# Kernel optimization log

Hardware: AMD Instinct MI355X
Metric: run time of the kernel (lower is better)

Reference implementation:

```python
import jax, jax.numpy as jnp
import numpy as np

N = 50000      # nodes
E = 800000     # directed edges
D = 128        # input_dim == hidden_dim
EL = 100000    # edges scored by decoder


def setup_inputs() -> dict:
    key = jax.random.key(0)
    ks = jax.random.split(key, 8)
    s = 1.0 / np.sqrt(D)  # glorot-ish scale
    return {
        "node_feature": jax.random.normal(ks[0], (N, D), jnp.float32),
        "W1": jax.random.normal(ks[1], (D, D), jnp.float32) * s,
        "b1": jnp.zeros((D,), jnp.float32),
        "W2": jax.random.normal(ks[2], (D, D), jnp.float32) * s,
        "b2": jnp.zeros((D,), jnp.float32),
        "W3": jax.random.normal(ks[3], (D, D), jnp.float32) * s,
        "b3": jnp.zeros((D,), jnp.float32),
        "edge_index": jax.random.randint(ks[4], (2, E), 0, N, dtype=jnp.int32),
        "edge_label_index": jax.random.randint(ks[5], (2, EL), 0, N, dtype=jnp.int32),
    }


def _gcn_conv(x, W, b, src, dst, norm, n):
    # x' = D^{-1/2} (A + I) D^{-1/2} (x W) + b   (PyG GCNConv semantics)
    h = x @ W                                   # [N, D]
    msg = h[src] * norm[:, None]                # gather + scale, [E+N, D]
    out = jax.ops.segment_sum(msg, dst, num_segments=n)  # scatter-add
    return out + b


def reference(node_feature, W1, b1, W2, b2, W3, b3, edge_index, edge_label_index):
    n = node_feature.shape[0]
    loop = jnp.arange(n, dtype=edge_index.dtype)
    src = jnp.concatenate([edge_index[0], loop])  # self-loops appended
    dst = jnp.concatenate([edge_index[1], loop])
    # symmetric normalization: deg over destinations (incl. self-loops)
    deg = jax.ops.segment_sum(jnp.ones_like(dst, dtype=node_feature.dtype), dst, num_segments=n)
    dinv = jax.lax.rsqrt(jnp.maximum(deg, 1.0))
    norm = dinv[src] * dinv[dst]                 # [E+N]

    x = jax.nn.relu(_gcn_conv(node_feature, W1, b1, src, dst, norm, n))
    x = jax.nn.relu(_gcn_conv(x, W2, b2, src, dst, norm, n))
    x = _gcn_conv(x, W3, b3, src, dst, norm, n)

    # dot-product edge decoder
    u = x[edge_label_index[0]]
    v = x[edge_label_index[1]]
    return jnp.sum(u * v, axis=-1)               # [EL] logits
```

## Files before the change

kernel.cpp:

```cpp
#include <hip/hip_runtime.h>
#include <hip/hip_bf16.h>
#include <hip/hip_fp16.h>

typedef _Float16 v8h __attribute__((ext_vector_type(8)));
typedef _Float16 v4h __attribute__((ext_vector_type(4)));
typedef float v4f __attribute__((ext_vector_type(4)));

__global__ __launch_bounds__(256) void hist_wswz(const int* __restrict__ dst,
                                                 int* __restrict__ histT, int E,
                                                 int histBlocks,
                                                 const float* __restrict__ W1,
                                                 const float* __restrict__ W2,
                                                 const float* __restrict__ W3,
                                                 __half* __restrict__ wfrag) {
    int tid = threadIdx.x;
    if (blockIdx.x >= histBlocks) {
        int o = (blockIdx.x - histBlocks) * 256 + tid;
        int w = o >> 14, r = o & 16383;
        const float* Ws = (w >= 3) ? W3 : ((w == 2) ? W2 : W1);
        float v = Ws[r];
        __half h;
        if (w == 1) {
            __half hv = __float2half_rn(v);
            h = __float2half_rn(v - __half2float(hv));
        } else {
            h = __float2half_rn(v);
        }
        int k = r >> 7, ncol = r & 127;
        int c = ncol >> 4, nl = ncol & 15;
        int s = k >> 5, quad = (k >> 3) & 3, j = k & 7;
        int di = ((c * 4 + s) * 64 + quad * 16 + nl) * 8 + j;
        wfrag[(size_t)w * 16384 + di] = h;
        return;
    }
    __shared__ int h[256];
    h[tid] = 0;
    __syncthreads();
    int base = blockIdx.x * 2048 + tid * 8;
    if (base + 7 < E) {
        int4 d0 = *(const int4*)&dst[base];
        int4 d1 = *(const int4*)&dst[base + 4];
        atomicAdd(&h[d0.x >> 8], 1);
        atomicAdd(&h[d0.y >> 8], 1);
        atomicAdd(&h[d0.z >> 8], 1);
        atomicAdd(&h[d0.w >> 8], 1);
        atomicAdd(&h[d1.x >> 8], 1);
        atomicAdd(&h[d1.y >> 8], 1);
        atomicAdd(&h[d1.z >> 8], 1);
        atomicAdd(&h[d1.w >> 8], 1);
    } else {
        for (int e = base; e < E; ++e) atomicAdd(&h[dst[e] >> 8], 1);
    }
    __syncthreads();
    histT[tid * 400 + blockIdx.x] = h[tid];
}

__global__ __launch_bounds__(512) void scan_bins(int* __restrict__ histT,
                                                 int* __restrict__ totals, int nb) {
    __shared__ int s[512];
    int b = blockIdx.x;
    int t = threadIdx.x;
    int v = (t < nb) ? histT[b * 400 + t] : 0;
    s[t] = v;
    __syncthreads();
    for (int off = 1; off < 512; off <<= 1) {
        int x = (t >= off) ? s[t - off] : 0;
        __syncthreads();
        s[t] += x;
        __syncthreads();
    }
    if (t < nb) histT[b * 400 + t] = s[t] - v;
    if (t == 511) totals[b] = s[511];
}

__global__ __launch_bounds__(256) void scan_totals(const int* __restrict__ totals,
                                                   int* __restrict__ binbase) {
    __shared__ int s[256];
    int t = threadIdx.x;
    int v = totals[t];
    s[t] = v;
    __syncthreads();
    for (int off = 1; off < 256; off <<= 1) {
        int x = (t >= off) ? s[t - off] : 0;
        __syncthreads();
        s[t] += x;
        __syncthreads();
    }
    binbase[t] = s[t] - v;
    if (t == 255) binbase[256] = s[255];
}

__global__ __launch_bounds__(256) void scat_gemm1(const int* __restrict__ src,
                                                  const int* __restrict__ dst,
                                                  const int* __restrict__ histT,
                                                  const int* __restrict__ binbase,
                                                  int* __restrict__ pairS, int E,
                                                  int scatBlocks,
                                                  const float* __restrict__ X,
                                                  const __half* __restrict__ wfrag,
                                                  __half* __restrict__ H, int Nrows) {
    int tid = threadIdx.x;
    if (blockIdx.x < scatBlocks) {
        __shared__ int pos[256];
        pos[tid] = binbase[tid] + histT[tid * 400 + blockIdx.x];
        __syncthreads();
        int base = blockIdx.x * 2048 + tid * 8;
        if (base + 7 < E) {
            int4 d0 = *(const int4*)&dst[base];
            int4 d1 = *(const int4*)&dst[base + 4];
            int4 s0 = *(const int4*)&src[base];
            int4 s1 = *(const int4*)&src[base + 4];
            int p0 = atomicAdd(&pos[d0.x >> 8], 1);
            int p1 = atomicAdd(&pos[d0.y >> 8], 1);
            int p2 = atomicAdd(&pos[d0.z >> 8], 1);
            int p3 = atomicAdd(&pos[d0.w >> 8], 1);
            int p4 = atomicAdd(&pos[d1.x >> 8], 1);
            int p5 = atomicAdd(&pos[d1.y >> 8], 1);
            int p6 = atomicAdd(&pos[d1.z >> 8], 1);
            int p7 = atomicAdd(&pos[d1.w >> 8], 1);
            pairS[p0] = ((d0.x & 255) << 16) | s0.x;
            pairS[p1] = ((d0.y & 255) << 16) | s0.y;
            pairS[p2] = ((d0.z & 255) << 16) | s0.z;
            pairS[p3] = ((d0.w & 255) << 16) | s0.w;
            pairS[p4] = ((d1.x & 255) << 16) | s1.x;
            pairS[p5] = ((d1.y & 255) << 16) | s1.y;
            pairS[p6] = ((d1.z & 255) << 16) | s1.z;
            pairS[p7] = ((d1.w & 255) << 16) | s1.w;
        } else {
            for (int e = base; e < E; ++e) {
                int d = dst[e];
                int p = atomicAdd(&pos[d >> 8], 1);
                pairS[p] = ((d & 255) << 16) | src[e];
            }
        }
        return;
    }
    int rowbase = (blockIdx.x - scatBlocks) * 64;
    int l = tid & 63;
    int wid = tid >> 6;
    int rb = wid * 16;
    int quad = l >> 4;
    int nn = l & 15;
    int gr = rowbase + rb + nn;
    v8h ah[4], al[4];
    if (gr < Nrows) {
        const float* Xr = &X[(size_t)gr * 128 + quad * 8];
#pragma unroll
        for (int k = 0; k < 4; ++k) {
            float4 f0 = *(const float4*)&Xr[k * 32];
            float4 f1 = *(const float4*)&Xr[k * 32 + 4];
            float ff[8] = {f0.x, f0.y, f0.z, f0.w, f1.x, f1.y, f1.z, f1.w};
            v8h h, lo;
#pragma unroll
            for (int m = 0; m < 8; ++m) {
                _Float16 hv = (_Float16)ff[m];
                h[m] = hv;
                lo[m] = (_Float16)(ff[m] - (float)hv);
            }
            ah[k] = h;
            al[k] = lo;
        }
    } else {
#pragma unroll
        for (int k = 0; k < 4; ++k) {
            v8h z;
#pragma unroll
            for (int m = 0; m < 8; ++m) z[m] = (_Float16)0.f;
            ah[k] = z;
            al[k] = z;
        }
    }
    const v8h* Wh = (const v8h*)wfrag;
    const v8h* Wl = (const v8h*)(wfrag + 16384);
    v4f acc[8] = {};
    v8h bh0 = Wh[0 * 64 + l];
    v8h bh1 = Wh[1 * 64 + l];
    v8h bh2 = Wh[2 * 64 + l];
    v8h bh3 = Wh[3 * 64 + l];
#pragma unroll
    for (int c = 0; c < 8; ++c) {
        v8h bl0 = Wl[(c * 4 + 0) * 64 + l];
        v8h bl1 = Wl[(c * 4 + 1) * 64 + l];
        v8h bl2 = Wl[(c * 4 + 2) * 64 + l];
        v8h bl3 = Wl[(c * 4 + 3) * 64 + l];
        acc[c] = __builtin_amdgcn_mfma_f32_16x16x32_f16(ah[0], bh0, acc[c], 0, 0, 0);
        acc[c] = __builtin_amdgcn_mfma_f32_16x16x32_f16(ah[1], bh1, acc[c], 0, 0, 0);
        acc[c] = __builtin_amdgcn_mfma_f32_16x16x32_f16(ah[2], bh2, acc[c], 0, 0, 0);
        acc[c] = __builtin_amdgcn_mfma_f32_16x16x32_f16(ah[3], bh3, acc[c], 0, 0, 0);
        acc[c] = __builtin_amdgcn_mfma_f32_16x16x32_f16(al[0], bh0, acc[c], 0, 0, 0);
        acc[c] = __builtin_amdgcn_mfma_f32_16x16x32_f16(al[1], bh1, acc[c], 0, 0, 0);
        acc[c] = __builtin_amdgcn_mfma_f32_16x16x32_f16(al[2], bh2, acc[c], 0, 0, 0);
        acc[c] = __builtin_amdgcn_mfma_f32_16x16x32_f16(al[3], bh3, acc[c], 0, 0, 0);
        v8h nh0, nh1, nh2, nh3;
        if (c < 7) {
            nh0 = Wh[((c + 1) * 4 + 0) * 64 + l];
            nh1 = Wh[((c + 1) * 4 + 1) * 64 + l];
            nh2 = Wh[((c + 1) * 4 + 2) * 64 + l];
            nh3 = Wh[((c + 1) * 4 + 3) * 64 + l];
        }
        acc[c] = __builtin_amdgcn_mfma_f32_16x16x32_f16(ah[0], bl0, acc[c], 0, 0, 0);
        acc[c] = __builtin_amdgcn_mfma_f32_16x16x32_f16(ah[1], bl1, acc[c], 0, 0, 0);
        acc[c] = __builtin_amdgcn_mfma_f32_16x16x32_f16(ah[2], bl2, acc[c], 0, 0, 0);
        acc[c] = __builtin_amdgcn_mfma_f32_16x16x32_f16(ah[3], bl3, acc[c], 0, 0, 0);
        if (c < 7) { bh0 = nh0; bh1 = nh1; bh2 = nh2; bh3 = nh3; }
    }
#pragma unroll
    for (int reg = 0; reg < 4; ++reg) {
        int grr = rowbase + rb + quad * 4 + reg;
        if (grr < Nrows) {
#pragma unroll
            for (int c = 0; c < 8; ++c)
                H[(size_t)grr * 128 + c * 16 + nn] = __float2half_rn(acc[c][reg]);
        }
    }
}

__global__ __launch_bounds__(256) void bucket_csr(const int* __restrict__ pairS,
                                                  const int* __restrict__ binbase,
                                                  int* __restrict__ rowptr,
                                                  float* __restrict__ dinv,
                                                  int* __restrict__ col, int N) {
    __shared__ int h[256];
    __shared__ int sc[256];
    __shared__ int cnt2[256];
    int b = blockIdx.x;
    int t = threadIdx.x;
    int ebeg = binbase[b], eend = binbase[b + 1];
    int base_sl = ebeg + b * 256;
    h[t] = 0;
    __syncthreads();
    for (int i = ebeg + t; i < eend; i += 256) atomicAdd(&h[pairS[i] >> 16], 1);
    __syncthreads();
    int deg = h[t];
    int node = b * 256 + t;
    bool valid = node < N;
    int v = valid ? (deg + 1) : 0;
    sc[t] = v;
    __syncthreads();
    for (int off = 1; off < 256; off <<= 1) {
        int x = (t >= off) ? sc[t - off] : 0;
        __syncthreads();
        sc[t] += x;
        __syncthreads();
    }
    int rs = base_sl + sc[t] - v;
    if (valid) {
        rowptr[node + 1] = base_sl + sc[t];
        dinv[node] = rsqrtf((float)(deg + 1));
        col[rs] = node;
        if (node == 0) rowptr[0] = 0;
    }
    cnt2[t] = rs + 1;
    __syncthreads();
    for (int i = ebeg + t; i < eend; i += 256) {
        int pv = pairS[i];
        int p = atomicAdd(&cnt2[pv >> 16], 1);
        col[p] = pv & 0xFFFF;
    }
}

__global__ __launch_bounds__(512, 8) void agg_gemm(const __half* __restrict__ Xs,
                                                   const float* __restrict__ dinv,
                                                   const int* __restrict__ rowptr,
                                                   const int* __restrict__ col,
                                                   const __half* __restrict__ wfrag,
                                                   const float* __restrict__ bias,
                                                   __half* __restrict__ Out,
                                                   int n, int finalLayer) {
    __shared__ __align__(16) _Float16 y[64][136];
    int tid = threadIdx.x;
    int rowbase = blockIdx.x * 64;
    {
        int grp = tid >> 4;
        int t = (tid & 15) * 8;
        for (int g = 0; g < 2; ++g) {
            int rr = g * 32 + grp;
            int node = rowbase + rr;
            float a[8] = {};
            if (node < n) {
                int beg = rowptr[node], end = rowptr[node + 1];
                int k = beg;
                for (; k + 4 <= end; k += 4) {
                    int s0 = col[k], s1 = col[k + 1], s2 = col[k + 2], s3 = col[k + 3];
                    uint4 r0 = *(const uint4*)&Xs[(size_t)s0 * 128 + t];
                    uint4 r1 = *(const uint4*)&Xs[(size_t)s1 * 128 + t];
                    uint4 r2 = *(const uint4*)&Xs[(size_t)s2 * 128 + t];
                    uint4 r3 = *(const uint4*)&Xs[(size_t)s3 * 128 + t];
                    const __half2* h0 = (const __half2*)&r0;
                    const __half2* h1 = (const __half2*)&r1;
                    const __half2* h2 = (const __half2*)&r2;
                    const __half2* h3 = (const __half2*)&r3;
#pragma unroll
                    for (int m = 0; m < 4; ++m) {
                        float2 f0 = __half22float2(h0[m]);
                        float2 f1 = __half22float2(h1[m]);
                        float2 f2 = __half22float2(h2[m]);
                        float2 f3 = __half22float2(h3[m]);
                        a[2 * m]     += (f0.x + f1.x) + (f2.x + f3.x);
                        a[2 * m + 1] += (f0.y + f1.y) + (f2.y + f3.y);
                    }
                }
                for (; k < end; ++k) {
                    uint4 r0 = *(const uint4*)&Xs[(size_t)col[k] * 128 + t];
                    const __half2* h0 = (const __half2*)&r0;
#pragma unroll
                    for (int m = 0; m < 4; ++m) {
                        float2 f0 = __half22float2(h0[m]);
                        a[2 * m] += f0.x;
                        a[2 * m + 1] += f0.y;
                    }
                }
                float dn = dinv[node];
#pragma unroll
                for (int m = 0; m < 8; ++m) a[m] *= dn;
            }
            v8h yv;
#pragma unroll
            for (int m = 0; m < 8; ++m) yv[m] = (_Float16)a[m];
            *(v8h*)&y[rr][t] = yv;
        }
    }
    __syncthreads();
    int l = tid & 63;
    int wid = tid >> 6;
    int rb = (wid >> 1) * 16;
    int ch = wid & 1;
    int quad = l >> 4;
    int nn = l & 15;
    v8h a0 = *(const v8h*)&y[rb + nn][0 * 32 + quad * 8];
    v8h a1 = *(const v8h*)&y[rb + nn][1 * 32 + quad * 8];
    v8h a2 = *(const v8h*)&y[rb + nn][2 * 32 + quad * 8];
    v8h a3 = *(const v8h*)&y[rb + nn][3 * 32 + quad * 8];
    const v8h* Wf = (const v8h*)wfrag;
    v4f acc[4] = {};
#pragma unroll
    for (int c = 0; c < 4; ++c) {
        int cc = ch * 4 + c;
        v8h b0 = Wf[(cc * 4 + 0) * 64 + l];
        v8h b1 = Wf[(cc * 4 + 1) * 64 + l];
        v8h b2 = Wf[(cc * 4 + 2) * 64 + l];
        v8h b3 = Wf[(cc * 4 + 3) * 64 + l];
        acc[c] = __builtin_amdgcn_mfma_f32_16x16x32_f16(a0, b0, acc[c], 0, 0, 0);
        acc[c] = __builtin_amdgcn_mfma_f32_16x16x32_f16(a1, b1, acc[c], 0, 0, 0);
        acc[c] = __builtin_amdgcn_mfma_f32_16x16x32_f16(a2, b2, acc[c], 0, 0, 0);
        acc[c] = __builtin_amdgcn_mfma_f32_16x16x32_f16(a3, b3, acc[c], 0, 0, 0);
    }
#pragma unroll
    for (int reg = 0; reg < 4; ++reg) {
        int gr = rowbase + rb + quad * 4 + reg;
        if (gr < n) {
            float dn = dinv[gr];
#pragma unroll
            for (int c = 0; c < 4; ++c) {
                int cc = ch * 4 + c;
                float z = acc[c][reg] + bias[cc * 16 + nn];
                if (!finalLayer) z = fmaxf(z, 0.f) * dn;
                Out[(size_t)gr * 128 + cc * 16 + nn] = __float2half_rn(z);
            }
        }
    }
}

__global__ __launch_bounds__(256, 8) void agg_h(const __half* __restrict__ H,
                                                const float* __restrict__ dinv,
                                                const int* __restrict__ rowptr,
                                                const int* __restrict__ col,
                                                const float* __restrict__ bias,
                                                __half* __restrict__ out, int n) {
    int node = blockIdx.x * 16 + (threadIdx.x >> 4);
    int t = (threadIdx.x & 15) * 8;
    if (node >= n) return;
    int beg = rowptr[node], end = rowptr[node + 1];
    float a[8] = {};
    int k = beg;
    for (; k + 4 <= end; k += 4) {
        int s0 = col[k], s1 = col[k + 1], s2 = col[k + 2], s3 = col[k + 3];
        float w0 = dinv[s0], w1 = dinv[s1], w2 = dinv[s2], w3 = dinv[s3];
        uint4 r0 = *(const uint4*)&H[(size_t)s0 * 128 + t];
        uint4 r1 = *(const uint4*)&H[(size_t)s1 * 128 + t];
        uint4 r2 = *(const uint4*)&H[(size_t)s2 * 128 + t];
        uint4 r3 = *(const uint4*)&H[(size_t)s3 * 128 + t];
        const __half2* h0 = (const __half2*)&r0;
        const __half2* h1 = (const __half2*)&r1;
        const __half2* h2 = (const __half2*)&r2;
        const __half2* h3 = (const __half2*)&r3;
#pragma unroll
        for (int m = 0; m < 4; ++m) {
            float2 f0 = __half22float2(h0[m]);
            float2 f1 = __half22float2(h1[m]);
            float2 f2 = __half22float2(h2[m]);
            float2 f3 = __half22float2(h3[m]);
            a[2 * m]     += f0.x * w0 + f1.x * w1 + f2.x * w2 + f3.x * w3;
            a[2 * m + 1] += f0.y * w0 + f1.y * w1 + f2.y * w2 + f3.y * w3;
        }
    }
    for (; k < end; ++k) {
        int s0 = col[k];
        float w0 = dinv[s0];
        uint4 r0 = *(const uint4*)&H[(size_t)s0 * 128 + t];
        const __half2* h0 = (const __half2*)&r0;
#pragma unroll
        for (int m = 0; m < 4; ++m) {
            float2 f0 = __half22float2(h0[m]);
            a[2 * m] += f0.x * w0;
            a[2 * m + 1] += f0.y * w0;
        }
    }
    float dn = dinv[node];
    float4 b0 = *(const float4*)&bias[t];
    float4 b1 = *(const float4*)&bias[t + 4];
    float r0 = fmaxf(a[0] * dn + b0.x, 0.f) * dn;
    float r1 = fmaxf(a[1] * dn + b0.y, 0.f) * dn;
    float r2 = fmaxf(a[2] * dn + b0.z, 0.f) * dn;
    float r3 = fmaxf(a[3] * dn + b0.w, 0.f) * dn;
    float r4 = fmaxf(a[4] * dn + b1.x, 0.f) * dn;
    float r5 = fmaxf(a[5] * dn + b1.y, 0.f) * dn;
    float r6 = fmaxf(a[6] * dn + b1.z, 0.f) * dn;
    float r7 = fmaxf(a[7] * dn + b1.w, 0.f) * dn;
    auto pk = [](float x, float y) { __half2 h = __floats2half2_rn(x, y); return *(unsigned int*)&h; };
    uint4 o = make_uint4(pk(r0, r1), pk(r2, r3), pk(r4, r5), pk(r6, r7));
    *(uint4*)&out[(size_t)node * 128 + t] = o;
}

__global__ __launch_bounds__(256) void decoder_h(const __half* __restrict__ X,
                                                 const int* __restrict__ eli,
                                                 float* __restrict__ out, int EL) {
    int e = blockIdx.x * 16 + (threadIdx.x >> 4);
    int lane = threadIdx.x & 15;
    if (e >= EL) return;
    int u = eli[e], v = eli[EL + e];
    uint4 ra = *(const uint4*)&X[(size_t)u * 128 + lane * 8];
    uint4 rb = *(const uint4*)&X[(size_t)v * 128 + lane * 8];
    const __half2* ha = (const __half2*)&ra;
    const __half2* hb = (const __half2*)&rb;
    float d = 0.f;
#pragma unroll
    for (int j = 0; j < 4; ++j) {
        float2 fa = __half22float2(ha[j]);
        float2 fb = __half22float2(hb[j]);
        d += fa.x * fb.x + fa.y * fb.y;
    }
#pragma unroll
    for (int off = 8; off > 0; off >>= 1) d += __shfl_xor(d, off);
    if (lane == 0) out[e] = d;
}

extern "C" void kernel_launch(void* const* d_in, const int* in_sizes, int n_in,
                              void* d_out, int out_size, void* d_ws, size_t ws_size,
                              hipStream_t stream) {
    const float* x0 = (const float*)d_in[0];
    const float* W1 = (const float*)d_in[1];
    const float* b1 = (const float*)d_in[2];
    const float* W2 = (const float*)d_in[3];
    const float* b2 = (const float*)d_in[4];
    const float* W3 = (const float*)d_in[5];
    const float* b3 = (const float*)d_in[6];
    const int* ei   = (const int*)d_in[7];
    const int* eli  = (const int*)d_in[8];
    float* out = (float*)d_out;

    const int D = 128;
    const int N  = in_sizes[0] / D;
    const int E  = in_sizes[7] / 2;
    const int EL = in_sizes[8] / 2;

    const int* src = ei;
    const int* dst = ei + E;

    char* ws = (char*)d_ws;
    size_t off = 0;
    auto alloc = [&](size_t bytes) -> void* {
        off = (off + 255) & ~(size_t)255;
        void* p = ws + off;
        off += bytes;
        return p;
    };
    int*    histT   = (int*)alloc((size_t)256 * 400 * sizeof(int));
    int*    totals  = (int*)alloc(256 * sizeof(int));
    int*    binbase = (int*)alloc(257 * sizeof(int));
    int*    pairS   = (int*)alloc((size_t)E * sizeof(int));
    int*    rowptr  = (int*)alloc((size_t)(N + 1) * sizeof(int));
    float*  dinv    = (float*)alloc((size_t)N * sizeof(float));
    int*    col     = (int*)alloc((size_t)(E + N) * sizeof(int));
    __half* wfrag   = (__half*)alloc((size_t)4 * 16384 * sizeof(__half));
    __half* hbuf    = (__half*)alloc((size_t)N * D * sizeof(__half));
    __half* xbuf    = (__half*)alloc((size_t)N * D * sizeof(__half));
    (void)ws_size;

    int histBlocks = (E + 2047) / 2048;
    int gemmGrid = (N + 63) / 64;
    int fusedGrid = (N + 63) / 64;
    int aggGrid  = (N + 15) / 16;
    int nbkt = (N + 255) / 256;

    hist_wswz<<<histBlocks + 256, 256, 0, stream>>>(dst, histT, E, histBlocks,
                                                    W1, W2, W3, wfrag);
    scan_bins<<<256, 512, 0, stream>>>(histT, totals, histBlocks);
    scan_totals<<<1, 256, 0, stream>>>(totals, binbase);
    scat_gemm1<<<histBlocks + gemmGrid, 256, 0, stream>>>(src, dst, histT, binbase,
                                                          pairS, E, histBlocks,
                                                          x0, wfrag, hbuf, N);
    bucket_csr<<<nbkt, 256, 0, stream>>>(pairS, binbase, rowptr, dinv, col, N);

    agg_h<<<aggGrid, 256, 0, stream>>>(hbuf, dinv, rowptr, col, b1, xbuf, N);
    agg_gemm<<<fusedGrid, 512, 0, stream>>>(xbuf, dinv, rowptr, col, wfrag + 2 * 16384, b2, hbuf, N, 0);
    agg_gemm<<<fusedGrid, 512, 0, stream>>>(hbuf, dinv, rowptr, col, wfrag + 3 * 16384, b3, xbuf, N, 1);

    decoder_h<<<(EL + 15) / 16, 256, 0, stream>>>(xbuf, eli, out, EL);
}
```

Before: 227.9 us.

## Sub-bin edge counting sort by source range within each destination bucket

The counting sort now bins edges by (dst>>8, coarse src range) with 8 source sub-bins per destination bucket, so edges inside each bucket end up partially ordered by source node. Column indices in the CSR should then show better gather locality for the H rows read during aggregation. The cost is an 8x larger histogram and scan (nbins up to about 1600 bins, 2048-entry shared arrays, a 1024-thread totals scan), plus extra src loads in the histogram kernel.

```diff
diff --git a/kernel.cpp b/kernel.cpp
--- a/kernel.cpp
+++ b/kernel.cpp
@@ -3,12 +3,12 @@
 #include <hip/hip_fp16.h>
 
 typedef _Float16 v8h __attribute__((ext_vector_type(8)));
-typedef _Float16 v4h __attribute__((ext_vector_type(4)));
 typedef float v4f __attribute__((ext_vector_type(4)));
 
 __global__ __launch_bounds__(256) void hist_wswz(const int* __restrict__ dst,
+                                                 const int* __restrict__ src,
                                                  int* __restrict__ histT, int E,
-                                                 int histBlocks,
+                                                 int histBlocks, int nbins, int srcShift,
                                                  const float* __restrict__ W1,
                                                  const float* __restrict__ W2,
                                                  const float* __restrict__ W3,
@@ -33,26 +33,29 @@
         wfrag[(size_t)w * 16384 + di] = h;
         return;
     }
-    __shared__ int h[256];
-    h[tid] = 0;
+    __shared__ int h[2048];
+    for (int i = tid; i < nbins; i += 256) h[i] = 0;
     __syncthreads();
     int base = blockIdx.x * 2048 + tid * 8;
     if (base + 7 < E) {
         int4 d0 = *(const int4*)&dst[base];
         int4 d1 = *(const int4*)&dst[base + 4];
-        atomicAdd(&h[d0.x >> 8], 1);
-        atomicAdd(&h[d0.y >> 8], 1);
-        atomicAdd(&h[d0.z >> 8], 1);
-        atomicAdd(&h[d0.w >> 8], 1);
-        atomicAdd(&h[d1.x >> 8], 1);
-        atomicAdd(&h[d1.y >> 8], 1);
-        atomicAdd(&h[d1.z >> 8], 1);
-        atomicAdd(&h[d1.w >> 8], 1);
+        int4 s0 = *(const int4*)&src[base];
+        int4 s1 = *(const int4*)&src[base + 4];
+        atomicAdd(&h[(d0.x >> 8) * 8 + (s0.x >> srcShift)], 1);
+        atomicAdd(&h[(d0.y >> 8) * 8 + (s0.y >> srcShift)], 1);
+        atomicAdd(&h[(d0.z >> 8) * 8 + (s0.z >> srcShift)], 1);
+        atomicAdd(&h[(d0.w >> 8) * 8 + (s0.w >> srcShift)], 1);
+        atomicAdd(&h[(d1.x >> 8) * 8 + (s1.x >> srcShift)], 1);
+        atomicAdd(&h[(d1.y >> 8) * 8 + (s1.y >> srcShift)], 1);
+        atomicAdd(&h[(d1.z >> 8) * 8 + (s1.z >> srcShift)], 1);
+        atomicAdd(&h[(d1.w >> 8) * 8 + (s1.w >> srcShift)], 1);
     } else {
-        for (int e = base; e < E; ++e) atomicAdd(&h[dst[e] >> 8], 1);
-    }
-    __syncthreads();
-    histT[tid * 400 + blockIdx.x] = h[tid];
+        for (int e = base; e < E; ++e)
+            atomicAdd(&h[(dst[e] >> 8) * 8 + (src[e] >> srcShift)], 1);
+    }
+    __syncthreads();
+    for (int i = tid; i < nbins; i += 256) histT[i * 400 + blockIdx.x] = h[i];
 }
 
 __global__ __launch_bounds__(512) void scan_bins(int* __restrict__ histT,
@@ -73,21 +76,26 @@
     if (t == 511) totals[b] = s[511];
 }
 
-__global__ __launch_bounds__(256) void scan_totals(const int* __restrict__ totals,
-                                                   int* __restrict__ binbase) {
-    __shared__ int s[256];
+__global__ __launch_bounds__(1024) void scan_totals(const int* __restrict__ totals,
+                                                    int* __restrict__ binbase, int nbins) {
+    __shared__ int s[1024];
     int t = threadIdx.x;
-    int v = totals[t];
-    s[t] = v;
-    __syncthreads();
-    for (int off = 1; off < 256; off <<= 1) {
+    int CH = (nbins + 1023) >> 10;
+    int beg = t * CH;
+    int end = min(beg + CH, nbins);
+    int sum = 0;
+    for (int i = beg; i < end; ++i) sum += totals[i];
+    s[t] = sum;
+    __syncthreads();
+    for (int off = 1; off < 1024; off <<= 1) {
         int x = (t >= off) ? s[t - off] : 0;
         __syncthreads();
         s[t] += x;
         __syncthreads();
     }
-    binbase[t] = s[t] - v;
-    if (t == 255) binbase[256] = s[255];
+    int run = s[t] - sum;
+    for (int i = beg; i < end; ++i) { binbase[i] = run; run += totals[i]; }
+    if (t == 1023) binbase[nbins] = s[1023];
 }
 
 __global__ __launch_bounds__(256) void scat_gemm1(const int* __restrict__ src,
@@ -95,14 +103,15 @@
                                                   const int* __restrict__ histT,
                                                   const int* __restrict__ binbase,
                                                   int* __restrict__ pairS, int E,
-                                                  int scatBlocks,
+                                                  int scatBlocks, int nbins, int srcShift,
                                                   const float* __restrict__ X,
                                                   const __half* __restrict__ wfrag,
                                                   __half* __restrict__ H, int Nrows) {
     int tid = threadIdx.x;
     if (blockIdx.x < scatBlocks) {
-        __shared__ int pos[256];
-        pos[tid] = binbase[tid] + histT[tid * 400 + blockIdx.x];
+        __shared__ int pos[2048];
+        for (int i = tid; i < nbins; i += 256)
+            pos[i] = binbase[i] + histT[i * 400 + blockIdx.x];
         __syncthreads();
         int base = blockIdx.x * 2048 + tid * 8;
         if (base + 7 < E) {
@@ -110,14 +119,14 @@
             int4 d1 = *(const int4*)&dst[base + 4];
             int4 s0 = *(const int4*)&src[base];
             int4 s1 = *(const int4*)&src[base + 4];
-            int p0 = atomicAdd(&pos[d0.x >> 8], 1);
-            int p1 = atomicAdd(&pos[d0.y >> 8], 1);
-            int p2 = atomicAdd(&pos[d0.z >> 8], 1);
-            int p3 = atomicAdd(&pos[d0.w >> 8], 1);
-            int p4 = atomicAdd(&pos[d1.x >> 8], 1);
-            int p5 = atomicAdd(&pos[d1.y >> 8], 1);
-            int p6 = atomicAdd(&pos[d1.z >> 8], 1);
-            int p7 = atomicAdd(&pos[d1.w >> 8], 1);
+            int p0 = atomicAdd(&pos[(d0.x >> 8) * 8 + (s0.x >> srcShift)], 1);
+            int p1 = atomicAdd(&pos[(d0.y >> 8) * 8 + (s0.y >> srcShift)], 1);
+            int p2 = atomicAdd(&pos[(d0.z >> 8) * 8 + (s0.z >> srcShift)], 1);
+            int p3 = atomicAdd(&pos[(d0.w >> 8) * 8 + (s0.w >> srcShift)], 1);
+            int p4 = atomicAdd(&pos[(d1.x >> 8) * 8 + (s1.x >> srcShift)], 1);
+            int p5 = atomicAdd(&pos[(d1.y >> 8) * 8 + (s1.y >> srcShift)], 1);
+            int p6 = atomicAdd(&pos[(d1.z >> 8) * 8 + (s1.z >> srcShift)], 1);
+            int p7 = atomicAdd(&pos[(d1.w >> 8) * 8 + (s1.w >> srcShift)], 1);
             pairS[p0] = ((d0.x & 255) << 16) | s0.x;
             pairS[p1] = ((d0.y & 255) << 16) | s0.y;
             pairS[p2] = ((d0.z & 255) << 16) | s0.z;
@@ -128,9 +137,9 @@
             pairS[p7] = ((d1.w & 255) << 16) | s1.w;
         } else {
             for (int e = base; e < E; ++e) {
-                int d = dst[e];
-                int p = atomicAdd(&pos[d >> 8], 1);
-                pairS[p] = ((d & 255) << 16) | src[e];
+                int d = dst[e], s = src[e];
+                int p = atomicAdd(&pos[(d >> 8) * 8 + (s >> srcShift)], 1);
+                pairS[p] = ((d & 255) << 16) | s;
             }
         }
         return;
@@ -225,7 +234,7 @@
     __shared__ int cnt2[256];
     int b = blockIdx.x;
     int t = threadIdx.x;
-    int ebeg = binbase[b], eend = binbase[b + 1];
+    int ebeg = binbase[b * 8], eend = binbase[b * 8 + 8];
     int base_sl = ebeg + b * 256;
     h[t] = 0;
     __syncthreads();
@@ -467,6 +476,15 @@
     const int* src = ei;
     const int* dst = ei + E;
 
+    int nbkt = (N + 255) / 256;
+    int nbins = nbkt * 8;
+    int srcShift = 0;
+    while (((N - 1) >> srcShift) >= 8) srcShift++;
+    int histBlocks = (E + 2047) / 2048;
+    int gemmGrid = (N + 63) / 64;
+    int fusedGrid = (N + 63) / 64;
+    int aggGrid  = (N + 15) / 16;
+
     char* ws = (char*)d_ws;
     size_t off = 0;
     auto alloc = [&](size_t bytes) -> void* {
@@ -475,9 +493,9 @@
         off += bytes;
         return p;
     };
-    int*    histT   = (int*)alloc((size_t)256 * 400 * sizeof(int));
-    int*    totals  = (int*)alloc(256 * sizeof(int));
-    int*    binbase = (int*)alloc(257 * sizeof(int));
+    int*    histT   = (int*)alloc((size_t)nbins * 400 * sizeof(int));
+    int*    totals  = (int*)alloc((size_t)nbins * sizeof(int));
+    int*    binbase = (int*)alloc((size_t)(nbins + 1) * sizeof(int));
     int*    pairS   = (int*)alloc((size_t)E * sizeof(int));
     int*    rowptr  = (int*)alloc((size_t)(N + 1) * sizeof(int));
     float*  dinv    = (float*)alloc((size_t)N * sizeof(float));
@@ -487,19 +505,13 @@
     __half* xbuf    = (__half*)alloc((size_t)N * D * sizeof(__half));
     (void)ws_size;
 
-    int histBlocks = (E + 2047) / 2048;
-    int gemmGrid = (N + 63) / 64;
-    int fusedGrid = (N + 63) / 64;
-    int aggGrid  = (N + 15) / 16;
-    int nbkt = (N + 255) / 256;
-
-    hist_wswz<<<histBlocks + 256, 256, 0, stream>>>(dst, histT, E, histBlocks,
-                                                    W1, W2, W3, wfrag);
-    scan_bins<<<256, 512, 0, stream>>>(histT, totals, histBlocks);
-    scan_totals<<<1, 256, 0, stream>>>(totals, binbase);
+    hist_wswz<<<histBlocks + 256, 256, 0, stream>>>(dst, src, histT, E, histBlocks,
+                                                    nbins, srcShift, W1, W2, W3, wfrag);
+    scan_bins<<<nbins, 512, 0, stream>>>(histT, totals, histBlocks);
+    scan_totals<<<1, 1024, 0, stream>>>(totals, binbase, nbins);
     scat_gemm1<<<histBlocks + gemmGrid, 256, 0, stream>>>(src, dst, histT, binbase,
-                                                          pairS, E, histBlocks,
-                                                          x0, wfrag, hbuf, N);
+                                                          pairS, E, histBlocks, nbins,
+                                                          srcShift, x0, wfrag, hbuf, N);
     bucket_csr<<<nbkt, 256, 0, stream>>>(pairS, binbase, rowptr, dinv, col, N);
 
     agg_h<<<aggGrid, 256, 0, stream>>>(hbuf, dinv, rowptr, col, b1, xbuf, N);
```

Result: slower. 238.6 us (+4.7%).

## Remap aggregation to 4 lanes per node looping over feature chunks

Applied to the files above, without the earlier changes.

Both aggregation kernels now give each node 4 threads that loop over four 32-column feature chunks, where before 16 threads covered all 128 columns in one pass. agg_gemm drops to 256 threads per block, and each wave computes all 8 output column tiles for its 16 rows instead of half of them. The aim is to cut per-node thread waste on low-degree rows and to amortize the rowptr/dinv loads. In exchange, each gather now moves only 64 contiguous bytes per node per chunk, the neighbor list is walked four times, and there is less memory-level parallelism per node.

```diff
diff --git a/kernel.cpp b/kernel.cpp
--- a/kernel.cpp
+++ b/kernel.cpp
@@ -3,7 +3,6 @@
 #include <hip/hip_fp16.h>
 
 typedef _Float16 v8h __attribute__((ext_vector_type(8)));
-typedef _Float16 v4h __attribute__((ext_vector_type(4)));
 typedef float v4f __attribute__((ext_vector_type(4)));
 
 __global__ __launch_bounds__(256) void hist_wswz(const int* __restrict__ dst,
@@ -259,7 +258,74 @@
     }
 }
 
-__global__ __launch_bounds__(512, 8) void agg_gemm(const __half* __restrict__ Xs,
+__global__ __launch_bounds__(256, 8) void agg_h(const __half* __restrict__ H,
+                                                const float* __restrict__ dinv,
+                                                const int* __restrict__ rowptr,
+                                                const int* __restrict__ col,
+                                                const float* __restrict__ bias,
+                                                __half* __restrict__ out, int n) {
+    int grp = threadIdx.x >> 2;
+    int lane = threadIdx.x & 3;
+    int node = blockIdx.x * 64 + grp;
+    int beg = 0, end = 0;
+    float dn = 0.f;
+    if (node < n) { beg = rowptr[node]; end = rowptr[node + 1]; dn = dinv[node]; }
+    auto pk = [](float x, float y) { __half2 h = __floats2half2_rn(x, y); return *(unsigned int*)&h; };
+    for (int q = 0; q < 4; ++q) {
+        int t = q * 32 + lane * 8;
+        float a[8] = {};
+        int k = beg;
+        for (; k + 4 <= end; k += 4) {
+            int s0 = col[k], s1 = col[k + 1], s2 = col[k + 2], s3 = col[k + 3];
+            float w0 = dinv[s0], w1 = dinv[s1], w2 = dinv[s2], w3 = dinv[s3];
+            uint4 r0 = *(const uint4*)&H[(size_t)s0 * 128 + t];
+            uint4 r1 = *(const uint4*)&H[(size_t)s1 * 128 + t];
+            uint4 r2 = *(const uint4*)&H[(size_t)s2 * 128 + t];
+            uint4 r3 = *(const uint4*)&H[(size_t)s3 * 128 + t];
+            const __half2* h0 = (const __half2*)&r0;
+            const __half2* h1 = (const __half2*)&r1;
+            const __half2* h2 = (const __half2*)&r2;
+            const __half2* h3 = (const __half2*)&r3;
+#pragma unroll
+            for (int m = 0; m < 4; ++m) {
+                float2 f0 = __half22float2(h0[m]);
+                float2 f1 = __half22float2(h1[m]);
+                float2 f2 = __half22float2(h2[m]);
+                float2 f3 = __half22float2(h3[m]);
+                a[2 * m]     += f0.x * w0 + f1.x * w1 + f2.x * w2 + f3.x * w3;
+                a[2 * m + 1] += f0.y * w0 + f1.y * w1 + f2.y * w2 + f3.y * w3;
+            }
+        }
+        for (; k < end; ++k) {
+            int s0 = col[k];
+            float w0 = dinv[s0];
+            uint4 r0 = *(const uint4*)&H[(size_t)s0 * 128 + t];
+            const __half2* h0 = (const __half2*)&r0;
+#pragma unroll
+            for (int m = 0; m < 4; ++m) {
+                float2 f0 = __half22float2(h0[m]);
+                a[2 * m] += f0.x * w0;
+                a[2 * m + 1] += f0.y * w0;
+            }
+        }
+        if (node < n) {
+            float4 b0 = *(const float4*)&bias[t];
+            float4 b1 = *(const float4*)&bias[t + 4];
+            float r0 = fmaxf(a[0] * dn + b0.x, 0.f) * dn;
+            float r1 = fmaxf(a[1] * dn + b0.y, 0.f) * dn;
+            float r2 = fmaxf(a[2] * dn + b0.z, 0.f) * dn;
+            float r3 = fmaxf(a[3] * dn + b0.w, 0.f) * dn;
+            float r4 = fmaxf(a[4] * dn + b1.x, 0.f) * dn;
+            float r5 = fmaxf(a[5] * dn + b1.y, 0.f) * dn;
+            float r6 = fmaxf(a[6] * dn + b1.z, 0.f) * dn;
+            float r7 = fmaxf(a[7] * dn + b1.w, 0.f) * dn;
+            uint4 o = make_uint4(pk(r0, r1), pk(r2, r3), pk(r4, r5), pk(r6, r7));
+            *(uint4*)&out[(size_t)node * 128 + t] = o;
+        }
+    }
+}
+
+__global__ __launch_bounds__(256, 8) void agg_gemm(const __half* __restrict__ Xs,
                                                    const float* __restrict__ dinv,
                                                    const int* __restrict__ rowptr,
                                                    const int* __restrict__ col,
@@ -271,60 +337,56 @@
     int tid = threadIdx.x;
     int rowbase = blockIdx.x * 64;
     {
-        int grp = tid >> 4;
-        int t = (tid & 15) * 8;
-        for (int g = 0; g < 2; ++g) {
-            int rr = g * 32 + grp;
-            int node = rowbase + rr;
+        int grp = tid >> 2;
+        int lane = tid & 3;
+        int node = rowbase + grp;
+        int beg = 0, end = 0;
+        float dn = 0.f;
+        if (node < n) { beg = rowptr[node]; end = rowptr[node + 1]; dn = dinv[node]; }
+        for (int q = 0; q < 4; ++q) {
+            int t = q * 32 + lane * 8;
             float a[8] = {};
-            if (node < n) {
-                int beg = rowptr[node], end = rowptr[node + 1];
-                int k = beg;
-                for (; k + 4 <= end; k += 4) {
-                    int s0 = col[k], s1 = col[k + 1], s2 = col[k + 2], s3 = col[k + 3];
-                    uint4 r0 = *(const uint4*)&Xs[(size_t)s0 * 128 + t];
-                    uint4 r1 = *(const uint4*)&Xs[(size_t)s1 * 128 + t];
-                    uint4 r2 = *(const uint4*)&Xs[(size_t)s2 * 128 + t];
-                    uint4 r3 = *(const uint4*)&Xs[(size_t)s3 * 128 + t];
-                    const __half2* h0 = (const __half2*)&r0;
-                    const __half2* h1 = (const __half2*)&r1;
-                    const __half2* h2 = (const __half2*)&r2;
-                    const __half2* h3 = (const __half2*)&r3;
-#pragma unroll
-                    for (int m = 0; m < 4; ++m) {
-                        float2 f0 = __half22float2(h0[m]);
-                        float2 f1 = __half22float2(h1[m]);
-                        float2 f2 = __half22float2(h2[m]);
-                        float2 f3 = __half22float2(h3[m]);
-                        a[2 * m]     += (f0.x + f1.x) + (f2.x + f3.x);
-                        a[2 * m + 1] += (f0.y + f1.y) + (f2.y + f3.y);
-                    }
+            int k = beg;
+            for (; k + 4 <= end; k += 4) {
+                int s0 = col[k], s1 = col[k + 1], s2 = col[k + 2], s3 = col[k + 3];
+                uint4 r0 = *(const uint4*)&Xs[(size_t)s0 * 128 + t];
+                uint4 r1 = *(const uint4*)&Xs[(size_t)s1 * 128 + t];
+                uint4 r2 = *(const uint4*)&Xs[(size_t)s2 * 128 + t];
+                uint4 r3 = *(const uint4*)&Xs[(size_t)s3 * 128 + t];
+                const __half2* h0 = (const __half2*)&r0;
+                const __half2* h1 = (const __half2*)&r1;
+                const __half2* h2 = (const __half2*)&r2;
+                const __half2* h3 = (const __half2*)&r3;
+#pragma unroll
+                for (int m = 0; m < 4; ++m) {
+                    float2 f0 = __half22float2(h0[m]);
+                    float2 f1 = __half22float2(h1[m]);
+                    float2 f2 = __half22float2(h2[m]);
+                    float2 f3 = __half22float2(h3[m]);
+                    a[2 * m]     += (f0.x + f1.x) + (f2.x + f3.x);
+                    a[2 * m + 1] += (f0.y + f1.y) + (f2.y + f3.y);
                 }
-                for (; k < end; ++k) {
-                    uint4 r0 = *(const uint4*)&Xs[(size_t)col[k] * 128 + t];
-                    const __half2* h0 = (const __half2*)&r0;
-#pragma unroll
-                    for (int m = 0; m < 4; ++m) {
-                        float2 f0 = __half22float2(h0[m]);
-                        a[2 * m] += f0.x;
-                        a[2 * m + 1] += f0.y;
-                    }
+            }
+            for (; k < end; ++k) {
+                uint4 r0 = *(const uint4*)&Xs[(size_t)col[k] * 128 + t];
+                const __half2* h0 = (const __half2*)&r0;
+#pragma unroll
+                for (int m = 0; m < 4; ++m) {
+                    float2 f0 = __half22float2(h0[m]);
+                    a[2 * m] += f0.x;
+                    a[2 * m + 1] += f0.y;
                 }
-                float dn = dinv[node];
-#pragma unroll
-                for (int m = 0; m < 8; ++m) a[m] *= dn;
             }
             v8h yv;
 #pragma unroll
-            for (int m = 0; m < 8; ++m) yv[m] = (_Float16)a[m];
-            *(v8h*)&y[rr][t] = yv;
+            for (int m = 0; m < 8; ++m) yv[m] = (_Float16)(a[m] * dn);
+            *(v8h*)&y[grp][t] = yv;
         }
     }
     __syncthreads();
     int l = tid & 63;
     int wid = tid >> 6;
-    int rb = (wid >> 1) * 16;
-    int ch = wid & 1;
+    int rb = wid * 16;
     int quad = l >> 4;
     int nn = l & 15;
     v8h a0 = *(const v8h*)&y[rb + nn][0 * 32 + quad * 8];
@@ -332,14 +394,13 @@
     v8h a2 = *(const v8h*)&y[rb + nn][2 * 32 + quad * 8];
     v8h a3 = *(const v8h*)&y[rb + nn][3 * 32 + quad * 8];
     const v8h* Wf = (const v8h*)wfrag;
-    v4f acc[4] = {};
-#pragma unroll
-    for (int c = 0; c < 4; ++c) {
-        int cc = ch * 4 + c;
-        v8h b0 = Wf[(cc * 4 + 0) * 64 + l];
-        v8h b1 = Wf[(cc * 4 + 1) * 64 + l];
-        v8h b2 = Wf[(cc * 4 + 2) * 64 + l];
-        v8h b3 = Wf[(cc * 4 + 3) * 64 + l];
+    v4f acc[8] = {};
+#pragma unroll
+    for (int c = 0; c < 8; ++c) {
+        v8h b0 = Wf[(c * 4 + 0) * 64 + l];
+        v8h b1 = Wf[(c * 4 + 1) * 64 + l];
+        v8h b2 = Wf[(c * 4 + 2) * 64 + l];
+        v8h b3 = Wf[(c * 4 + 3) * 64 + l];
         acc[c] = __builtin_amdgcn_mfma_f32_16x16x32_f16(a0, b0, acc[c], 0, 0, 0);
         acc[c] = __builtin_amdgcn_mfma_f32_16x16x32_f16(a1, b1, acc[c], 0, 0, 0);
         acc[c] = __builtin_amdgcn_mfma_f32_16x16x32_f16(a2, b2, acc[c], 0, 0, 0);
@@ -351,75 +412,13 @@
         if (gr < n) {
             float dn = dinv[gr];
 #pragma unroll
-            for (int c = 0; c < 4; ++c) {
-                int cc = ch * 4 + c;
-                float z = acc[c][reg] + bias[cc * 16 + nn];
+            for (int c = 0; c < 8; ++c) {
+                float z = acc[c][reg] + bias[c * 16 + nn];
                 if (!finalLayer) z = fmaxf(z, 0.f) * dn;
-                Out[(size_t)gr * 128 + cc * 16 + nn] = __float2half_rn(z);
-            }
-        }
-    }
-}
-
-__global__ __launch_bounds__(256, 8) void agg_h(const __half* __restrict__ H,
-                                                const float* __restrict__ dinv,
-                                                const int* __restrict__ rowptr,
-                                                const int* __restrict__ col,
-                                                const float* __restrict__ bias,
-                                                __half* __restrict__ out, int n) {
-    int node = blockIdx.x * 16 + (threadIdx.x >> 4);
-    int t = (threadIdx.x & 15) * 8;
-    if (node >= n) return;
-    int beg = rowptr[node], end = rowptr[node + 1];
-    float a[8] = {};
-    int k = beg;
-    for (; k + 4 <= end; k += 4) {
-        int s0 = col[k], s1 = col[k + 1], s2 = col[k + 2], s3 = col[k + 3];
-        float w0 = dinv[s0], w1 = dinv[s1], w2 = dinv[s2], w3 = dinv[s3];
-        uint4 r0 = *(const uint4*)&H[(size_t)s0 * 128 + t];
-        uint4 r1 = *(const uint4*)&H[(size_t)s1 * 128 + t];
-        uint4 r2 = *(const uint4*)&H[(size_t)s2 * 128 + t];
-        uint4 r3 = *(const uint4*)&H[(size_t)s3 * 128 + t];
-        const __half2* h0 = (const __half2*)&r0;
-        const __half2* h1 = (const __half2*)&r1;
-        const __half2* h2 = (const __half2*)&r2;
-        const __half2* h3 = (const __half2*)&r3;
-#pragma unroll
-        for (int m = 0; m < 4; ++m) {
-            float2 f0 = __half22float2(h0[m]);
-            float2 f1 = __half22float2(h1[m]);
-            float2 f2 = __half22float2(h2[m]);
-            float2 f3 = __half22float2(h3[m]);
-            a[2 * m]     += f0.x * w0 + f1.x * w1 + f2.x * w2 + f3.x * w3;
-            a[2 * m + 1] += f0.y * w0 + f1.y * w1 + f2.y * w2 + f3.y * w3;
-        }
-    }
-    for (; k < end; ++k) {
-        int s0 = col[k];
-        float w0 = dinv[s0];
-        uint4 r0 = *(const uint4*)&H[(size_t)s0 * 128 + t];
-        const __half2* h0 = (const __half2*)&r0;
-#pragma unroll
-        for (int m = 0; m < 4; ++m) {
-            float2 f0 = __half22float2(h0[m]);
-            a[2 * m] += f0.x * w0;
-            a[2 * m + 1] += f0.y * w0;
-        }
-    }
-    float dn = dinv[node];
-    float4 b0 = *(const float4*)&bias[t];
-    float4 b1 = *(const float4*)&bias[t + 4];
-    float r0 = fmaxf(a[0] * dn + b0.x, 0.f) * dn;
-    float r1 = fmaxf(a[1] * dn + b0.y, 0.f) * dn;
-    float r2 = fmaxf(a[2] * dn + b0.z, 0.f) * dn;
-    float r3 = fmaxf(a[3] * dn + b0.w, 0.f) * dn;
-    float r4 = fmaxf(a[4] * dn + b1.x, 0.f) * dn;
-    float r5 = fmaxf(a[5] * dn + b1.y, 0.f) * dn;
-    float r6 = fmaxf(a[6] * dn + b1.z, 0.f) * dn;
-    float r7 = fmaxf(a[7] * dn + b1.w, 0.f) * dn;
-    auto pk = [](float x, float y) { __half2 h = __floats2half2_rn(x, y); return *(unsigned int*)&h; };
-    uint4 o = make_uint4(pk(r0, r1), pk(r2, r3), pk(r4, r5), pk(r6, r7));
-    *(uint4*)&out[(size_t)node * 128 + t] = o;
+                Out[(size_t)gr * 128 + c * 16 + nn] = __float2half_rn(z);
+            }
+        }
+    }
 }
 
 __global__ __launch_bounds__(256) void decoder_h(const __half* __restrict__ X,
@@ -489,8 +488,7 @@
 
     int histBlocks = (E + 2047) / 2048;
     int gemmGrid = (N + 63) / 64;
-    int fusedGrid = (N + 63) / 64;
-    int aggGrid  = (N + 15) / 16;
+    int aggGrid  = (N + 63) / 64;
     int nbkt = (N + 255) / 256;
 
     hist_wswz<<<histBlocks + 256, 256, 0, stream>>>(dst, histT, E, histBlocks,
@@ -503,8 +501,8 @@
     bucket_csr<<<nbkt, 256, 0, stream>>>(pairS, binbase, rowptr, dinv, col, N);
 
     agg_h<<<aggGrid, 256, 0, stream>>>(hbuf, dinv, rowptr, col, b1, xbuf, N);
-    agg_gemm<<<fusedGrid, 512, 0, stream>>>(xbuf, dinv, rowptr, col, wfrag + 2 * 16384, b2, hbuf, N, 0);
-    agg_gemm<<<fusedGrid, 512, 0, stream>>>(hbuf, dinv, rowptr, col, wfrag + 3 * 16384, b3, xbuf, N, 1);
+    agg_gemm<<<aggGrid, 256, 0, stream>>>(xbuf, dinv, rowptr, col, wfrag + 2 * 16384, b2, hbuf, N, 0);
+    agg_gemm<<<aggGrid, 256, 0, stream>>>(hbuf, dinv, rowptr, col, wfrag + 3 * 16384, b3, xbuf, N, 1);
 
     decoder_h<<<(EL + 15) / 16, 256, 0, stream>>>(xbuf, eli, out, EL);
 }
```

Result: slower. 287.5 us (+26.2%).
